# Optimization experiments

Measured on AMD Instinct MI355X. Metric: run time of the kernel, lower is better.

Reference implementation:

```python
import jax, jax.numpy as jnp
import numpy as np
from jax import lax

# Static module config (matches init_kwargs)
KH, KW = 3, 3
SH, SW = 1, 1
PH, PW = 1, 1
DH, DW = 1, 1
DG = 1           # deformable groups
GROUPS = 1


def setup_inputs() -> dict:
    key = jax.random.key(0)
    k1, k2, k3 = jax.random.split(key, 3)
    B, C, H, W = 8, 256, 64, 64
    Co = 256
    K = KH * KW
    x = jax.random.normal(k1, (B, C, H, W), dtype=jnp.float32)
    # offset/mask conv weight: (2+1)*DG*K = 27 output channels; small so offsets are a few pixels
    w_offset = jax.random.normal(k2, (3 * DG * K, C, KH, KW), dtype=jnp.float32) * 0.05
    # main conv weight, uniform(-stdv, stdv) per reset_parameters
    stdv = 1.0 / np.sqrt(C * KH * KW)
    w_conv = jax.random.uniform(k3, (Co, C, KH, KW), dtype=jnp.float32, minval=-stdv, maxval=stdv)
    return {"input_feat": x, "w_offset": w_offset, "w_conv": w_conv}


def _bilinear_gather(x, py, px):
    """x: (B, DG, Cg, H, W); py/px: (B, DG, K, Ho, Wo) float sample coords.
    Returns sampled values (B, DG, Cg, K, Ho, Wo) with zero padding outside."""
    B, dg, Cg, H, W = x.shape
    _, _, K, Ho, Wo = py.shape
    xf = x.reshape(B, dg, Cg, H * W)

    y0 = jnp.floor(py)
    x0 = jnp.floor(px)
    ly = py - y0
    lx = px - x0
    y0i = y0.astype(jnp.int32)
    x0i = x0.astype(jnp.int32)
    y1i = y0i + 1
    x1i = x0i + 1

    def gather(yi, xi):
        valid = (yi >= 0) & (yi < H) & (xi >= 0) & (xi < W)
        idx = jnp.clip(yi, 0, H - 1) * W + jnp.clip(xi, 0, W - 1)  # (B,dg,K,Ho,Wo)
        idx_f = idx.reshape(B, dg, K * Ho * Wo)
        g = jax.vmap(jax.vmap(lambda f, i: jnp.take(f, i, axis=1)))(xf, idx_f)
        return g.reshape(B, dg, Cg, K, Ho, Wo), valid

    g00, v00 = gather(y0i, x0i)
    g01, v01 = gather(y0i, x1i)
    g10, v10 = gather(y1i, x0i)
    g11, v11 = gather(y1i, x1i)

    w00 = ((1 - ly) * (1 - lx) * v00)[:, :, None]
    w01 = ((1 - ly) * lx * v01)[:, :, None]
    w10 = (ly * (1 - lx) * v10)[:, :, None]
    w11 = (ly * lx * v11)[:, :, None]
    return g00 * w00 + g01 * w01 + g10 * w10 + g11 * w11


def _deform_conv(x, w_offset, w_conv):
    B, C, H, W = x.shape
    Co = w_conv.shape[0]
    K = KH * KW
    dn = ("NCHW", "OIHW", "NCHW")

    # offset/mask branch (regular conv)
    om = lax.conv_general_dilated(x, w_offset, (SH, SW), ((PH, PH), (PW, PW)),
                                  rhs_dilation=(DH, DW), dimension_numbers=dn)
    Ho, Wo = om.shape[2], om.shape[3]
    off_y = om[:, : DG * K].reshape(B, DG, K, Ho, Wo)
    off_x = om[:, DG * K: 2 * DG * K].reshape(B, DG, K, Ho, Wo)
    mask = jax.nn.sigmoid(om[:, 2 * DG * K:]).reshape(B, DG, 1, K, Ho, Wo)

    # base sampling grid
    oy = jnp.arange(Ho) * SH - PH                 # (Ho,)
    ox = jnp.arange(Wo) * SW - PW                 # (Wo,)
    ky = (jnp.arange(KH) * DH)[:, None].repeat(KW, 1).reshape(K)  # (K,)
    kx = (jnp.arange(KW) * DW)[None, :].repeat(KH, 0).reshape(K)  # (K,)
    py = ky[None, None, :, None, None] + oy[None, None, None, :, None] + off_y
    px = kx[None, None, :, None, None] + ox[None, None, None, None, :] + off_x

    xg = x.reshape(B, DG, C // DG, H, W)
    sampled = _bilinear_gather(xg, py, px) * mask  # (B,DG,Cg,K,Ho,Wo)

    cols = sampled.reshape(B, C, K, Ho * Wo)
    wk = w_conv.reshape(Co, C, K)
    out = jnp.einsum("bckn,ock->bon", cols, wk)
    return out.reshape(B, Co, Ho, Wo)


def reference(input_feat, w_offset, w_conv):
    return _deform_conv(input_feat, w_offset, w_conv)
```

## Files before the change

kernel.cpp:

```cpp
#include <hip/hip_runtime.h>
#include <hip/hip_bf16.h>

typedef float f32x4 __attribute__((ext_vector_type(4)));
typedef unsigned int u32x4 __attribute__((ext_vector_type(4)));
typedef __bf16 bf16x8 __attribute__((ext_vector_type(8)));

#define NSP 4096
#define KTOT 2304

static __device__ __forceinline__ float bflo(unsigned u) {
  return __builtin_bit_cast(float, u << 16);
}
static __device__ __forceinline__ float bfhi(unsigned u) {
  return __builtin_bit_cast(float, u & 0xffff0000u);
}
static __device__ __forceinline__ unsigned short bfbits(float f) {
  return __builtin_bit_cast(unsigned short, (__bf16)f);
}
static __device__ __forceinline__ unsigned packbf2(float f0, float f1) {
  return (unsigned)bfbits(f0) | ((unsigned)bfbits(f1) << 16);
}
static __device__ __forceinline__ float bf16f(unsigned short h) {
  return __builtin_bit_cast(float, (unsigned)h << 16);
}

static __device__ __forceinline__ void dma16(const unsigned short* g, unsigned short* l) {
  __builtin_amdgcn_global_load_lds(
      (const __attribute__((address_space(1))) unsigned int*)g,
      (__attribute__((address_space(3))) unsigned int*)l, 16, 0, 0);
}

__global__ __launch_bounds__(256) void k_nhwc(const float* __restrict__ x,
                                              unsigned short* __restrict__ XH) {
  const int by = blockIdx.x;
  const int t = threadIdx.x;
  const int xw = t & 63;
  const int cq = t >> 6;
  const float* xp = x + (((by >> 6) * 256 * 64 + (by & 63)) * 64 + xw);
  unsigned short* oh = XH + (by * 64 + xw) * 256;
#pragma unroll
  for (int j8 = 0; j8 < 8; ++j8) {
    const int c0 = cq * 64 + j8 * 8;
    u32x4 vh;
#pragma unroll
    for (int d = 0; d < 4; ++d) {
      float f0 = xp[(c0 + 2 * d) * 4096];
      float f1 = xp[(c0 + 2 * d + 1) * 4096];
      vh[d] = packbf2(f0, f1);
    }
    *(u32x4*)(oh + c0) = vh;
  }
}

__global__ void k_wprep_all(const float* __restrict__ wc, const float* __restrict__ wof,
                            unsigned short* __restrict__ AWL,
                            unsigned short* __restrict__ AF) {
  int idx = blockIdx.x * 256 + threadIdx.x;
  if (idx < 589824) {
    int ks = idx / 16384;
    int e = idx - ks * 16384;
    int row = e >> 6;
    int se = e & 63;
    int offb = (se * 2) ^ ((row & 7) << 4);
    int col = ks * 64 + (offb >> 1);
    int c = col & 255, tap = col >> 8;
    AWL[idx] = bfbits(wc[(row * 256 + c) * 9 + tap]);
  } else {
    int j = idx - 589824;
    if (j < 147456) {
      int skc = j >> 11;
      int r = j & 2047;
      int fi = r >> 9;
      int lane = (r >> 3) & 63;
      int e = r & 7;
      int ks = skc >> 1, kc = skc & 1;
      int tap = ks >> 2, q = ks & 3;
      int mr = lane & 15, ko = (lane >> 4) * 8;
      int m = (fi & 1) * 16 + mr;
      int gcol = tap * 256 + q * 64 + ko + kc * 32 + e;
      int c = gcol & 255;
      int t = gcol >> 8;
      float v = (m < 27) ? wof[(m * 256 + c) * 9 + t] : 0.f;
      unsigned short h = bfbits(v);
      AF[j] = (fi >> 1) ? bfbits(v - bf16f(h)) : h;
    }
  }
}

__global__ __launch_bounds__(256) void k_offc2(const unsigned short* __restrict__ AF,
                                               const unsigned short* __restrict__ XH,
                                               f32x4* __restrict__ W4,
                                               unsigned* __restrict__ C4) {
  __shared__ u32x4 ldsq[1024];
  unsigned char* ldsbase = (unsigned char*)ldsq;
  float* lds32 = (float*)ldsq;

  const int tid = threadIdx.x;
  const int bid = blockIdx.x;
  const int b = bid & 7;
  const int y = bid >> 3;
  const int l = tid & 63;
  const int w = tid >> 6;

  const unsigned short* xb = XH + b * (64 * 64 * 256);
  const int sp = tid >> 2;
  const int qtr = tid & 3;
  const unsigned swb = (unsigned)(sp & 7) << 4;
  const int col = w * 16 + (l & 15);
  const unsigned swc = (unsigned)(col & 7) << 4;

  f32x4 acc0 = (f32x4){0.f, 0.f, 0.f, 0.f};
  f32x4 acc1 = (f32x4){0.f, 0.f, 0.f, 0.f};
  u32x4 v0, v1;

  {
    const int yy = y - 1;
    const int xx = sp - 1;
    const bool valid = ((unsigned)yy < 64u) & ((unsigned)xx < 64u);
    const int yyc = min(max(yy, 0), 63), xxc = min(max(xx, 0), 63);
    const unsigned short* src = xb + ((yyc * 64 + xxc) * 256 + qtr * 16);
    u32x4 z = (u32x4){0u, 0u, 0u, 0u};
    v0 = valid ? *(const u32x4*)src : z;
    v1 = valid ? *(const u32x4*)(src + 8) : z;
    *(u32x4*)(ldsbase + (unsigned)sp * 128u + (((unsigned)(qtr * 32)) ^ swb)) = v0;
    *(u32x4*)(ldsbase + (unsigned)sp * 128u + (((unsigned)(qtr * 32 + 16)) ^ swb)) = v1;
  }

  for (int ks = 0; ks < 36; ++ks) {
    unsigned char* ldsB = ldsbase + (ks & 1) * 8192;
    unsigned char* ldsBn = ldsbase + ((ks & 1) ^ 1) * 8192;
    const bool pf = (ks + 1 < 36);

    if (pf) {
      int tap = (ks + 1) >> 2, q = (ks + 1) & 3;
      int yy = y + tap / 3 - 1, xx = sp + tap % 3 - 1;
      bool valid = ((unsigned)yy < 64u) & ((unsigned)xx < 64u);
      int yyc = min(max(yy, 0), 63), xxc = min(max(xx, 0), 63);
      const unsigned short* src = xb + ((yyc * 64 + xxc) * 256 + q * 64 + qtr * 16);
      u32x4 z = (u32x4){0u, 0u, 0u, 0u};
      v0 = valid ? *(const u32x4*)src : z;
      v1 = valid ? *(const u32x4*)(src + 8) : z;
    }

    asm volatile("s_waitcnt lgkmcnt(0)" ::: "memory");
    __builtin_amdgcn_s_barrier();

    const unsigned short* af = AF + ks * 4096;
#pragma unroll
    for (int kc = 0; kc < 2; ++kc) {
      bf16x8 ah0 = *(const bf16x8*)(af + kc * 2048 + l * 8);
      bf16x8 ah1 = *(const bf16x8*)(af + kc * 2048 + 512 + l * 8);
      bf16x8 al0 = *(const bf16x8*)(af + kc * 2048 + 1024 + l * 8);
      bf16x8 al1 = *(const bf16x8*)(af + kc * 2048 + 1536 + l * 8);
      bf16x8 bh = *(const bf16x8*)(ldsB + (unsigned)col * 128u +
                                   (((unsigned)(kc * 64 + (l >> 4) * 16)) ^ swc));
      acc0 = __builtin_amdgcn_mfma_f32_16x16x32_bf16(ah0, bh, acc0, 0, 0, 0);
      acc1 = __builtin_amdgcn_mfma_f32_16x16x32_bf16(ah1, bh, acc1, 0, 0, 0);
      acc0 = __builtin_amdgcn_mfma_f32_16x16x32_bf16(al0, bh, acc0, 0, 0, 0);
      acc1 = __builtin_amdgcn_mfma_f32_16x16x32_bf16(al1, bh, acc1, 0, 0, 0);
    }

    if (pf) {
      *(u32x4*)(ldsBn + (unsigned)sp * 128u + (((unsigned)(qtr * 32)) ^ swb)) = v0;
      *(u32x4*)(ldsBn + (unsigned)sp * 128u + (((unsigned)(qtr * 32 + 16)) ^ swb)) = v1;
    }
  }

  __syncthreads();
#pragma unroll
  for (int mf = 0; mf < 2; ++mf) {
    f32x4 a = mf ? acc1 : acc0;
#pragma unroll
    for (int r = 0; r < 4; ++r) {
      int m = mf * 16 + (l >> 4) * 4 + r;
      int px = w * 16 + (l & 15);
      lds32[m * 64 + px] = a[r];
    }
  }
  __syncthreads();

#pragma unroll
  for (int it = 0; it < 3; ++it) {
    int idx = tid + it * 256;
    if (idx < 9 * 64) {
      int k = idx >> 6, px = idx & 63;
      float oy = lds32[k * 64 + px];
      float ox = lds32[(9 + k) * 64 + px];
      float lg = lds32[(18 + k) * 64 + px];
      int s = y * 64 + px;
      float py = oy + (float)y - 1.f + (float)(k / 3);
      float pxf = ox + (float)px - 1.f + (float)(k % 3);
      float mk = 1.f / (1.f + __expf(-lg));

      float y0f = floorf(py), x0f = floorf(pxf);
      float ly = py - y0f, lx = pxf - x0f;
      int y0 = (int)y0f, x0 = (int)x0f;
      int y1 = y0 + 1, x1 = x0 + 1;
      float omy = 1.f - ly, omx = 1.f - lx;
      bool y0v = (unsigned)y0 < 64u, y1v = (unsigned)y1 < 64u;
      bool x0v = (unsigned)x0 < 64u, x1v = (unsigned)x1 < 64u;
      f32x4 wv;
      wv[0] = (y0v && x0v) ? omy * omx * mk : 0.f;
      wv[1] = (y0v && x1v) ? omy * lx * mk : 0.f;
      wv[2] = (y1v && x0v) ? ly * omx * mk : 0.f;
      wv[3] = (y1v && x1v) ? ly * lx * mk : 0.f;
      int y0c = min(max(y0, 0), 63), y1c = min(max(y1, 0), 63);
      int x0c = min(max(x0, 0), 63), x1c = min(max(x1, 0), 63);
      unsigned p00 = (unsigned)(y0c * 64 + x0c);
      unsigned p11 = (unsigned)(y1c * 64 + x1c);
      int ci = (b * 9 + k) * NSP + s;
      W4[ci] = wv;
      C4[ci] = p00 | (p11 << 16);
    }
  }
}

struct Bld16 {
  u32x4 g00a, g00b, g01a, g01b, g10a, g10b, g11a, g11b;
  f32x4 wv;
};

static __device__ __forceinline__ void loadMeta(const f32x4* __restrict__ W4,
                                                const unsigned* __restrict__ C4,
                                                int b, int k, int s,
                                                f32x4& wv, unsigned& c4) {
  int ci = (b * 9 + k) * NSP + s;
  wv = W4[ci];
  c4 = C4[ci];
}

static __device__ __forceinline__ void loadCorners(const unsigned short* __restrict__ xb,
                                                   f32x4 wv, unsigned c4, int c0, int bc,
                                                   Bld16& r) {
  r.wv = wv;
  unsigned p00 = c4 & 0xffffu, p11 = c4 >> 16;
  unsigned p01 = (p00 & ~63u) | (p11 & 63u);
  unsigned p10 = (p11 & ~63u) | (p00 & 63u);
  const unsigned short* base = xb + (c0 + bc);
  const unsigned short* q00 = base + (p00 << 8);
  const unsigned short* q01 = base + (p01 << 8);
  const unsigned short* q10 = base + (p10 << 8);
  const unsigned short* q11 = base + (p11 << 8);
  r.g00a = *(const u32x4*)q00;
  r.g00b = *(const u32x4*)(q00 + 8);
  r.g01a = *(const u32x4*)q01;
  r.g01b = *(const u32x4*)(q01 + 8);
  r.g10a = *(const u32x4*)q10;
  r.g10b = *(const u32x4*)(q10 + 8);
  r.g11a = *(const u32x4*)q11;
  r.g11b = *(const u32x4*)(q11 + 8);
}

static __device__ __forceinline__ void blendB16(const Bld16& r, u32x4& o0, u32x4& o1) {
#pragma unroll
  for (int d = 0; d < 4; ++d) {
    float a0 = r.wv[0] * bflo(r.g00a[d]) + r.wv[1] * bflo(r.g01a[d]) +
               r.wv[2] * bflo(r.g10a[d]) + r.wv[3] * bflo(r.g11a[d]);
    float a1 = r.wv[0] * bfhi(r.g00a[d]) + r.wv[1] * bfhi(r.g01a[d]) +
               r.wv[2] * bfhi(r.g10a[d]) + r.wv[3] * bfhi(r.g11a[d]);
    o0[d] = packbf2(a0, a1);
    float b0 = r.wv[0] * bflo(r.g00b[d]) + r.wv[1] * bflo(r.g01b[d]) +
               r.wv[2] * bflo(r.g10b[d]) + r.wv[3] * bflo(r.g11b[d]);
    float b1 = r.wv[0] * bfhi(r.g00b[d]) + r.wv[1] * bfhi(r.g01b[d]) +
               r.wv[2] * bfhi(r.g10b[d]) + r.wv[3] * bfhi(r.g11b[d]);
    o1[d] = packbf2(b0, b1);
  }
}

__global__ __launch_bounds__(512) void k_gemm(const unsigned short* __restrict__ AWL,
                                              const unsigned short* __restrict__ XH,
                                              const f32x4* __restrict__ W4,
                                              const unsigned* __restrict__ C4v,
                                              float* __restrict__ out) {
  __shared__ u32x4 lds2[2][3072];
  unsigned char* ldsbase = (unsigned char*)lds2;

  const int tid = threadIdx.x;
  const int bid = blockIdx.x;
  const int b = bid & 7;
  const int s0 = (bid >> 3) * 128;

  const int l = tid & 63;
  const int w = tid >> 6;
  const int wm = (w >> 1) * 64;
  const int wn = (w & 1) * 64;

  const int bn = tid >> 2;
  const int bc = (tid & 3) * 16;
  const int s = s0 + bn;
  const unsigned swb = (unsigned)(bn & 7) << 4;
  const unsigned short* xb = XH + b * (64 * 64 * 256);

  f32x4 acc[4][4];
#pragma unroll
  for (int i = 0; i < 4; ++i)
#pragma unroll
    for (int j = 0; j < 4; ++j) acc[i][j] = (f32x4){0.f, 0.f, 0.f, 0.f};

  f32x4 mwvA, mwvB;
  unsigned mc4A, mc4B;
  Bld16 bldA, bldB;

  loadMeta(W4, C4v, b, 0, s, mwvA, mc4A);
  loadMeta(W4, C4v, b, 0, s, mwvB, mc4B);
  {
    const unsigned short* g0 = AWL + (w * 4) * 512 + l * 8;
#pragma unroll
    for (int k = 0; k < 4; ++k)
      dma16(g0 + k * 512, (unsigned short*)(ldsbase + (unsigned)(w * 4 + k) * 1024u));
  }
  loadCorners(xb, mwvA, mc4A, 0, bc, bldA);
  loadMeta(W4, C4v, b, 0, s, mwvA, mc4A);
  {
    u32x4 o0, o1;
    blendB16(bldA, o0, o1);
    unsigned char* ldsB = ldsbase + 32768;
    const unsigned bbase = (unsigned)bn * 128u;
    *(u32x4*)(ldsB + bbase + (((unsigned)(bc * 2)) ^ swb)) = o0;
    *(u32x4*)(ldsB + bbase + (((unsigned)(bc * 2 + 16)) ^ swb)) = o1;
  }
  loadCorners(xb, mwvB, mc4B, 64, bc, bldB);

  auto mfma_half = [&](unsigned char* ldsA, unsigned char* ldsB, int H) {
    bf16x8 af[4], bfr[4];
    const unsigned co = (unsigned)(H * 64 + ((l >> 4) * 16));
#pragma unroll
    for (int i = 0; i < 4; ++i) {
      int row = wm + i * 16 + (l & 15);
      af[i] = *(const bf16x8*)(ldsA + (unsigned)row * 128u +
                               (co ^ ((unsigned)(row & 7) << 4)));
    }
#pragma unroll
    for (int j = 0; j < 4; ++j) {
      int col = wn + j * 16 + (l & 15);
      bfr[j] = *(const bf16x8*)(ldsB + (unsigned)col * 128u +
                                (co ^ ((unsigned)(col & 7) << 4)));
    }
#pragma unroll
    for (int i = 0; i < 4; ++i)
#pragma unroll
      for (int j = 0; j < 4; ++j)
        acc[i][j] = __builtin_amdgcn_mfma_f32_16x16x32_bf16(af[i], bfr[j],
                                                            acc[i][j], 0, 0, 0);
  };

  auto gstep = [&](int KS, Bld16& bldI, f32x4& mwvI, unsigned& mc4I,
                   f32x4& mwvO, unsigned& mc4O, Bld16& bldU) {
    const int cur = KS & 1;
    unsigned char* ldsA = ldsbase + cur * 49152;
    unsigned char* ldsB = ldsA + 32768;
    unsigned char* ldsAn = ldsbase + (cur ^ 1) * 49152;
    unsigned char* ldsBn = ldsAn + 32768;

    __syncthreads();

    if (KS + 1 < 36) {
      const unsigned short* g0 = AWL + (KS + 1) * 16384 + (w * 4) * 512 + l * 8;
#pragma unroll
      for (int k = 0; k < 4; ++k)
        dma16(g0 + k * 512, (unsigned short*)(ldsAn + (unsigned)(w * 4 + k) * 1024u));
    }

    __builtin_amdgcn_s_setprio(1);
    mfma_half(ldsA, ldsB, 0);
    __builtin_amdgcn_s_setprio(0);

    if (KS + 2 < 36)
      loadCorners(xb, mwvI, mc4I, ((KS + 2) & 3) << 6, bc, bldI);
    if (KS + 3 < 36)
      loadMeta(W4, C4v, b, (KS + 3) >> 2, s, mwvO, mc4O);

    __builtin_amdgcn_s_setprio(1);
    mfma_half(ldsA, ldsB, 1);
    __builtin_amdgcn_s_setprio(0);

    if (KS + 1 < 36) {
      u32x4 o0, o1;
      blendB16(bldU, o0, o1);
      const unsigned bbase = (unsigned)bn * 128u;
      *(u32x4*)(ldsBn + bbase + (((unsigned)(bc * 2)) ^ swb)) = o0;
      *(u32x4*)(ldsBn + bbase + (((unsigned)(bc * 2 + 16)) ^ swb)) = o1;
    }
  };

  for (int ks2 = 0; ks2 < 36; ks2 += 2) {
    gstep(ks2, bldA, mwvA, mc4A, mwvB, mc4B, bldB);
    gstep(ks2 + 1, bldB, mwvB, mc4B, mwvA, mc4A, bldA);
  }

  const int cn2 = l & 15;
  const int r0 = (l >> 4) * 4;
#pragma unroll
  for (int i = 0; i < 4; ++i) {
#pragma unroll
    for (int j = 0; j < 4; ++j) {
      int sc = s0 + wn + j * 16 + cn2;
#pragma unroll
      for (int r = 0; r < 4; ++r) {
        int o = wm + i * 16 + r0 + r;
        out[((b * 256 + o) << 12) + sc] = acc[i][j][r];
      }
    }
  }
}

extern "C" void kernel_launch(void* const* d_in, const int* in_sizes, int n_in,
                              void* d_out, int out_size, void* d_ws, size_t ws_size,
                              hipStream_t stream) {
  const float* x = (const float*)d_in[0];
  const float* wof = (const float*)d_in[1];
  const float* wc = (const float*)d_in[2];
  float* out = (float*)d_out;
  char* ws = (char*)d_ws;

  unsigned short* XH = (unsigned short*)(ws);
  unsigned short* AWL = (unsigned short*)(ws + 16777216);
  unsigned short* AF = (unsigned short*)(ws + 17956864);
  f32x4* W4 = (f32x4*)(ws + 18251776);
  unsigned* C4 = (unsigned*)(ws + 22970368);

  k_nhwc<<<512, 256, 0, stream>>>(x, XH);
  k_wprep_all<<<2880, 256, 0, stream>>>(wc, wof, AWL, AF);
  k_offc2<<<512, 256, 0, stream>>>(AF, XH, W4, C4);
  k_gemm<<<256, 512, 0, stream>>>(AWL, XH, W4, C4, out);
}
```

Baseline: 114.6 us.

## Split GEMM K dimension across two blocks with atomic accumulation

Splits the 36-step K loop of the deformable-conv GEMM into two halves handled by separate blocks, doubling the grid from 256 to 512 blocks so the 256-CU device is better filled. The output is zeroed with a memset and partial sums are combined with float atomicAdd. The B tile now uses a single LDS buffer guarded by an extra barrier, which shrinks LDS use to allow more blocks per CU. The cost is atomic traffic on the output, an extra memset, one more barrier per step, and nondeterministic summation order.

```diff
diff --git a/kernel.cpp b/kernel.cpp
--- a/kernel.cpp
+++ b/kernel.cpp
@@ -267,18 +267,20 @@
   }
 }
 
-__global__ __launch_bounds__(512) void k_gemm(const unsigned short* __restrict__ AWL,
-                                              const unsigned short* __restrict__ XH,
-                                              const f32x4* __restrict__ W4,
-                                              const unsigned* __restrict__ C4v,
-                                              float* __restrict__ out) {
-  __shared__ u32x4 lds2[2][3072];
+__global__ __launch_bounds__(512, 4) void k_gemm(const unsigned short* __restrict__ AWL,
+                                                 const unsigned short* __restrict__ XH,
+                                                 const f32x4* __restrict__ W4,
+                                                 const unsigned* __restrict__ C4v,
+                                                 float* __restrict__ out) {
+  __shared__ u32x4 lds2[5120];
   unsigned char* ldsbase = (unsigned char*)lds2;
+  unsigned char* ldsB = ldsbase + 65536;
 
   const int tid = threadIdx.x;
   const int bid = blockIdx.x;
   const int b = bid & 7;
-  const int s0 = (bid >> 3) * 128;
+  const int s0 = ((bid >> 3) & 31) * 128;
+  const int kb = (bid >> 8) * 18;
 
   const int l = tid & 63;
   const int w = tid >> 6;
@@ -301,27 +303,26 @@
   unsigned mc4A, mc4B;
   Bld16 bldA, bldB;
 
-  loadMeta(W4, C4v, b, 0, s, mwvA, mc4A);
-  loadMeta(W4, C4v, b, 0, s, mwvB, mc4B);
+  loadMeta(W4, C4v, b, kb >> 2, s, mwvA, mc4A);
+  loadMeta(W4, C4v, b, (kb + 1) >> 2, s, mwvB, mc4B);
   {
-    const unsigned short* g0 = AWL + (w * 4) * 512 + l * 8;
+    const unsigned short* g0 = AWL + kb * 16384 + (w * 4) * 512 + l * 8;
 #pragma unroll
     for (int k = 0; k < 4; ++k)
       dma16(g0 + k * 512, (unsigned short*)(ldsbase + (unsigned)(w * 4 + k) * 1024u));
   }
-  loadCorners(xb, mwvA, mc4A, 0, bc, bldA);
-  loadMeta(W4, C4v, b, 0, s, mwvA, mc4A);
+  loadCorners(xb, mwvA, mc4A, (kb & 3) << 6, bc, bldA);
+  loadMeta(W4, C4v, b, (kb + 2) >> 2, s, mwvA, mc4A);
   {
     u32x4 o0, o1;
     blendB16(bldA, o0, o1);
-    unsigned char* ldsB = ldsbase + 32768;
     const unsigned bbase = (unsigned)bn * 128u;
     *(u32x4*)(ldsB + bbase + (((unsigned)(bc * 2)) ^ swb)) = o0;
     *(u32x4*)(ldsB + bbase + (((unsigned)(bc * 2 + 16)) ^ swb)) = o1;
   }
-  loadCorners(xb, mwvB, mc4B, 64, bc, bldB);
-
-  auto mfma_half = [&](unsigned char* ldsA, unsigned char* ldsB, int H) {
+  loadCorners(xb, mwvB, mc4B, ((kb + 1) & 3) << 6, bc, bldB);
+
+  auto mfma_half = [&](unsigned char* ldsA, int H) {
     bf16x8 af[4], bfr[4];
     const unsigned co = (unsigned)(H * 64 + ((l >> 4) * 16));
 #pragma unroll
@@ -346,44 +347,45 @@
 
   auto gstep = [&](int KS, Bld16& bldI, f32x4& mwvI, unsigned& mc4I,
                    f32x4& mwvO, unsigned& mc4O, Bld16& bldU) {
-    const int cur = KS & 1;
-    unsigned char* ldsA = ldsbase + cur * 49152;
-    unsigned char* ldsB = ldsA + 32768;
-    unsigned char* ldsAn = ldsbase + (cur ^ 1) * 49152;
-    unsigned char* ldsBn = ldsAn + 32768;
+    const int G = kb + KS;
+    unsigned char* ldsA = ldsbase + (KS & 1) * 32768;
+    unsigned char* ldsAn = ldsbase + ((KS & 1) ^ 1) * 32768;
 
     __syncthreads();
 
-    if (KS + 1 < 36) {
-      const unsigned short* g0 = AWL + (KS + 1) * 16384 + (w * 4) * 512 + l * 8;
+    if (KS + 1 < 18) {
+      const unsigned short* g0 = AWL + (G + 1) * 16384 + (w * 4) * 512 + l * 8;
 #pragma unroll
       for (int k = 0; k < 4; ++k)
         dma16(g0 + k * 512, (unsigned short*)(ldsAn + (unsigned)(w * 4 + k) * 1024u));
     }
 
     __builtin_amdgcn_s_setprio(1);
-    mfma_half(ldsA, ldsB, 0);
+    mfma_half(ldsA, 0);
     __builtin_amdgcn_s_setprio(0);
 
-    if (KS + 2 < 36)
-      loadCorners(xb, mwvI, mc4I, ((KS + 2) & 3) << 6, bc, bldI);
-    if (KS + 3 < 36)
-      loadMeta(W4, C4v, b, (KS + 3) >> 2, s, mwvO, mc4O);
+    if (KS + 2 < 18)
+      loadCorners(xb, mwvI, mc4I, ((G + 2) & 3) << 6, bc, bldI);
+    if (KS + 3 < 18)
+      loadMeta(W4, C4v, b, (G + 3) >> 2, s, mwvO, mc4O);
 
     __builtin_amdgcn_s_setprio(1);
-    mfma_half(ldsA, ldsB, 1);
+    mfma_half(ldsA, 1);
     __builtin_amdgcn_s_setprio(0);
 
-    if (KS + 1 < 36) {
+    asm volatile("s_waitcnt lgkmcnt(0)" ::: "memory");
+    __builtin_amdgcn_s_barrier();
+
+    if (KS + 1 < 18) {
       u32x4 o0, o1;
       blendB16(bldU, o0, o1);
       const unsigned bbase = (unsigned)bn * 128u;
-      *(u32x4*)(ldsBn + bbase + (((unsigned)(bc * 2)) ^ swb)) = o0;
-      *(u32x4*)(ldsBn + bbase + (((unsigned)(bc * 2 + 16)) ^ swb)) = o1;
+      *(u32x4*)(ldsB + bbase + (((unsigned)(bc * 2)) ^ swb)) = o0;
+      *(u32x4*)(ldsB + bbase + (((unsigned)(bc * 2 + 16)) ^ swb)) = o1;
     }
   };
 
-  for (int ks2 = 0; ks2 < 36; ks2 += 2) {
+  for (int ks2 = 0; ks2 < 18; ks2 += 2) {
     gstep(ks2, bldA, mwvA, mc4A, mwvB, mc4B, bldB);
     gstep(ks2 + 1, bldB, mwvB, mc4B, mwvA, mc4A, bldA);
   }
@@ -398,7 +400,7 @@
 #pragma unroll
       for (int r = 0; r < 4; ++r) {
         int o = wm + i * 16 + r0 + r;
-        out[((b * 256 + o) << 12) + sc] = acc[i][j][r];
+        atomicAdd(&out[((b * 256 + o) << 12) + sc], acc[i][j][r]);
       }
     }
   }
@@ -419,8 +421,9 @@
   f32x4* W4 = (f32x4*)(ws + 18251776);
   unsigned* C4 = (unsigned*)(ws + 22970368);
 
+  hipMemsetAsync(d_out, 0, (size_t)out_size * 4, stream);
   k_nhwc<<<512, 256, 0, stream>>>(x, XH);
   k_wprep_all<<<2880, 256, 0, stream>>>(wc, wof, AWL, AF);
   k_offc2<<<512, 256, 0, stream>>>(AF, XH, W4, C4);
-  k_gemm<<<256, 512, 0, stream>>>(AWL, XH, W4, C4, out);
-}
+  k_gemm<<<512, 512, 0, stream>>>(AWL, XH, W4, C4, out);
+}
```

Result: slower. 407.4 us (+255.6%).

## Split gemm block into MFMA consumer waves and dedicated gather-blend producer waves

Applied to the files above, without the earlier changes.

The fused deformable-gather GEMM now launches 768 threads per block: 8 waves only run MFMA on the LDS tiles and issue the weight DMA, while 4 extra producer waves gather the bilinear corners, blend them, and write the next B tile into double-buffered LDS. The goal is to take the gather latency and blend ALU work off the MFMA waves so the two overlap through warp specialization. The cost is a larger block with more registers per block, a producer that now covers 32 channels per thread with a shallower one-step prefetch, and a reorganised LDS layout.

```diff
diff --git a/kernel.cpp b/kernel.cpp
--- a/kernel.cpp
+++ b/kernel.cpp
@@ -215,81 +215,33 @@
   }
 }
 
-struct Bld16 {
-  u32x4 g00a, g00b, g01a, g01b, g10a, g10b, g11a, g11b;
-  f32x4 wv;
-};
-
-static __device__ __forceinline__ void loadMeta(const f32x4* __restrict__ W4,
-                                                const unsigned* __restrict__ C4,
-                                                int b, int k, int s,
-                                                f32x4& wv, unsigned& c4) {
-  int ci = (b * 9 + k) * NSP + s;
-  wv = W4[ci];
-  c4 = C4[ci];
-}
-
-static __device__ __forceinline__ void loadCorners(const unsigned short* __restrict__ xb,
-                                                   f32x4 wv, unsigned c4, int c0, int bc,
-                                                   Bld16& r) {
-  r.wv = wv;
-  unsigned p00 = c4 & 0xffffu, p11 = c4 >> 16;
-  unsigned p01 = (p00 & ~63u) | (p11 & 63u);
-  unsigned p10 = (p11 & ~63u) | (p00 & 63u);
-  const unsigned short* base = xb + (c0 + bc);
-  const unsigned short* q00 = base + (p00 << 8);
-  const unsigned short* q01 = base + (p01 << 8);
-  const unsigned short* q10 = base + (p10 << 8);
-  const unsigned short* q11 = base + (p11 << 8);
-  r.g00a = *(const u32x4*)q00;
-  r.g00b = *(const u32x4*)(q00 + 8);
-  r.g01a = *(const u32x4*)q01;
-  r.g01b = *(const u32x4*)(q01 + 8);
-  r.g10a = *(const u32x4*)q10;
-  r.g10b = *(const u32x4*)(q10 + 8);
-  r.g11a = *(const u32x4*)q11;
-  r.g11b = *(const u32x4*)(q11 + 8);
-}
-
-static __device__ __forceinline__ void blendB16(const Bld16& r, u32x4& o0, u32x4& o1) {
-#pragma unroll
-  for (int d = 0; d < 4; ++d) {
-    float a0 = r.wv[0] * bflo(r.g00a[d]) + r.wv[1] * bflo(r.g01a[d]) +
-               r.wv[2] * bflo(r.g10a[d]) + r.wv[3] * bflo(r.g11a[d]);
-    float a1 = r.wv[0] * bfhi(r.g00a[d]) + r.wv[1] * bfhi(r.g01a[d]) +
-               r.wv[2] * bfhi(r.g10a[d]) + r.wv[3] * bfhi(r.g11a[d]);
-    o0[d] = packbf2(a0, a1);
-    float b0 = r.wv[0] * bflo(r.g00b[d]) + r.wv[1] * bflo(r.g01b[d]) +
-               r.wv[2] * bflo(r.g10b[d]) + r.wv[3] * bflo(r.g11b[d]);
-    float b1 = r.wv[0] * bfhi(r.g00b[d]) + r.wv[1] * bfhi(r.g01b[d]) +
-               r.wv[2] * bfhi(r.g10b[d]) + r.wv[3] * bfhi(r.g11b[d]);
-    o1[d] = packbf2(b0, b1);
-  }
-}
-
-__global__ __launch_bounds__(512) void k_gemm(const unsigned short* __restrict__ AWL,
-                                              const unsigned short* __restrict__ XH,
-                                              const f32x4* __restrict__ W4,
-                                              const unsigned* __restrict__ C4v,
-                                              float* __restrict__ out) {
-  __shared__ u32x4 lds2[2][3072];
+__global__ __launch_bounds__(768, 3) void k_gemm(const unsigned short* __restrict__ AWL,
+                                                 const unsigned short* __restrict__ XH,
+                                                 const f32x4* __restrict__ W4,
+                                                 const unsigned* __restrict__ C4v,
+                                                 float* __restrict__ out) {
+  __shared__ u32x4 lds2[6144];
   unsigned char* ldsbase = (unsigned char*)lds2;
+  unsigned char* ldsBbase = ldsbase + 65536;
 
   const int tid = threadIdx.x;
   const int bid = blockIdx.x;
   const int b = bid & 7;
   const int s0 = (bid >> 3) * 128;
+  const unsigned short* xb = XH + b * (64 * 64 * 256);
+
+  const bool isProd = tid >= 512;
 
   const int l = tid & 63;
   const int w = tid >> 6;
   const int wm = (w >> 1) * 64;
   const int wn = (w & 1) * 64;
 
-  const int bn = tid >> 2;
-  const int bc = (tid & 3) * 16;
-  const int s = s0 + bn;
-  const unsigned swb = (unsigned)(bn & 7) << 4;
-  const unsigned short* xb = XH + b * (64 * 64 * 256);
+  const int pt = tid - 512;
+  const int px = pt >> 1;
+  const int chb = (pt & 1) * 32;
+  const int ps = s0 + px;
+  const unsigned swb = (unsigned)(px & 7) << 4;
 
   f32x4 acc[4][4];
 #pragma unroll
@@ -297,108 +249,154 @@
 #pragma unroll
     for (int j = 0; j < 4; ++j) acc[i][j] = (f32x4){0.f, 0.f, 0.f, 0.f};
 
-  f32x4 mwvA, mwvB;
-  unsigned mc4A, mc4B;
-  Bld16 bldA, bldB;
-
-  loadMeta(W4, C4v, b, 0, s, mwvA, mc4A);
-  loadMeta(W4, C4v, b, 0, s, mwvB, mc4B);
-  {
+  u32x4 c00[4], c01[4], c10[4], c11[4];
+  f32x4 mwv;
+  unsigned mc4 = 0u;
+
+  if (!isProd) {
     const unsigned short* g0 = AWL + (w * 4) * 512 + l * 8;
 #pragma unroll
     for (int k = 0; k < 4; ++k)
       dma16(g0 + k * 512, (unsigned short*)(ldsbase + (unsigned)(w * 4 + k) * 1024u));
-  }
-  loadCorners(xb, mwvA, mc4A, 0, bc, bldA);
-  loadMeta(W4, C4v, b, 0, s, mwvA, mc4A);
-  {
-    u32x4 o0, o1;
-    blendB16(bldA, o0, o1);
-    unsigned char* ldsB = ldsbase + 32768;
-    const unsigned bbase = (unsigned)bn * 128u;
-    *(u32x4*)(ldsB + bbase + (((unsigned)(bc * 2)) ^ swb)) = o0;
-    *(u32x4*)(ldsB + bbase + (((unsigned)(bc * 2 + 16)) ^ swb)) = o1;
-  }
-  loadCorners(xb, mwvB, mc4B, 64, bc, bldB);
-
-  auto mfma_half = [&](unsigned char* ldsA, unsigned char* ldsB, int H) {
-    bf16x8 af[4], bfr[4];
-    const unsigned co = (unsigned)(H * 64 + ((l >> 4) * 16));
+  } else {
+    {
+      int ci = (b * 9 + 0) * NSP + ps;
+      mwv = W4[ci];
+      mc4 = C4v[ci];
+    }
+    {
+      unsigned p00 = mc4 & 0xffffu, p11 = mc4 >> 16;
+      unsigned p01 = (p00 & ~63u) | (p11 & 63u);
+      unsigned p10 = (p11 & ~63u) | (p00 & 63u);
+      const unsigned short* base = xb + chb;
+      const unsigned short* q00 = base + (p00 << 8);
+      const unsigned short* q01 = base + (p01 << 8);
+      const unsigned short* q10 = base + (p10 << 8);
+      const unsigned short* q11 = base + (p11 << 8);
+#pragma unroll
+      for (int q = 0; q < 4; ++q) {
+        c00[q] = *(const u32x4*)(q00 + q * 8);
+        c01[q] = *(const u32x4*)(q01 + q * 8);
+        c10[q] = *(const u32x4*)(q10 + q * 8);
+        c11[q] = *(const u32x4*)(q11 + q * 8);
+      }
+#pragma unroll
+      for (int q = 0; q < 4; ++q) {
+        u32x4 o;
+#pragma unroll
+        for (int d = 0; d < 4; ++d) {
+          float a0 = mwv[0] * bflo(c00[q][d]) + mwv[1] * bflo(c01[q][d]) +
+                     mwv[2] * bflo(c10[q][d]) + mwv[3] * bflo(c11[q][d]);
+          float a1 = mwv[0] * bfhi(c00[q][d]) + mwv[1] * bfhi(c01[q][d]) +
+                     mwv[2] * bfhi(c10[q][d]) + mwv[3] * bfhi(c11[q][d]);
+          o[d] = packbf2(a0, a1);
+        }
+        *(u32x4*)(ldsBbase + (unsigned)px * 128u +
+                  (((unsigned)(chb * 2 + q * 16)) ^ swb)) = o;
+      }
+    }
+    {
+      int ci = (b * 9 + 0) * NSP + ps;
+      mwv = W4[ci];
+      mc4 = C4v[ci];
+    }
+  }
+
+  for (int t = 0; t < 36; ++t) {
+    __syncthreads();
+
+    if (!isProd) {
+      if (t + 1 < 36) {
+        const unsigned short* g0 = AWL + (t + 1) * 16384 + (w * 4) * 512 + l * 8;
+        unsigned char* ldsAn = ldsbase + ((t + 1) & 1) * 32768;
+#pragma unroll
+        for (int k = 0; k < 4; ++k)
+          dma16(g0 + k * 512, (unsigned short*)(ldsAn + (unsigned)(w * 4 + k) * 1024u));
+      }
+      unsigned char* ldsA = ldsbase + (t & 1) * 32768;
+      unsigned char* ldsB = ldsBbase + (t & 1) * 16384;
+      __builtin_amdgcn_s_setprio(1);
+#pragma unroll
+      for (int H = 0; H < 2; ++H) {
+        bf16x8 af[4], bfr[4];
+        const unsigned co = (unsigned)(H * 64 + ((l >> 4) * 16));
+#pragma unroll
+        for (int i = 0; i < 4; ++i) {
+          int row = wm + i * 16 + (l & 15);
+          af[i] = *(const bf16x8*)(ldsA + (unsigned)row * 128u +
+                                   (co ^ ((unsigned)(row & 7) << 4)));
+        }
+#pragma unroll
+        for (int j = 0; j < 4; ++j) {
+          int col = wn + j * 16 + (l & 15);
+          bfr[j] = *(const bf16x8*)(ldsB + (unsigned)col * 128u +
+                                    (co ^ ((unsigned)(col & 7) << 4)));
+        }
+#pragma unroll
+        for (int i = 0; i < 4; ++i)
+#pragma unroll
+          for (int j = 0; j < 4; ++j)
+            acc[i][j] = __builtin_amdgcn_mfma_f32_16x16x32_bf16(af[i], bfr[j],
+                                                                acc[i][j], 0, 0, 0);
+      }
+      __builtin_amdgcn_s_setprio(0);
+    } else {
+      f32x4 wvS = mwv;
+      if (t + 1 < 36) {
+        unsigned p00 = mc4 & 0xffffu, p11 = mc4 >> 16;
+        unsigned p01 = (p00 & ~63u) | (p11 & 63u);
+        unsigned p10 = (p11 & ~63u) | (p00 & 63u);
+        const unsigned short* base = xb + (((t + 1) & 3) << 6) + chb;
+        const unsigned short* q00 = base + (p00 << 8);
+        const unsigned short* q01 = base + (p01 << 8);
+        const unsigned short* q10 = base + (p10 << 8);
+        const unsigned short* q11 = base + (p11 << 8);
+#pragma unroll
+        for (int q = 0; q < 4; ++q) {
+          c00[q] = *(const u32x4*)(q00 + q * 8);
+          c01[q] = *(const u32x4*)(q01 + q * 8);
+          c10[q] = *(const u32x4*)(q10 + q * 8);
+          c11[q] = *(const u32x4*)(q11 + q * 8);
+        }
+      }
+      if (t + 2 < 36) {
+        int ci = (b * 9 + ((t + 2) >> 2)) * NSP + ps;
+        mwv = W4[ci];
+        mc4 = C4v[ci];
+      }
+      if (t + 1 < 36) {
+        unsigned char* ldsBn = ldsBbase + ((t + 1) & 1) * 16384;
+#pragma unroll
+        for (int q = 0; q < 4; ++q) {
+          u32x4 o;
+#pragma unroll
+          for (int d = 0; d < 4; ++d) {
+            float a0 = wvS[0] * bflo(c00[q][d]) + wvS[1] * bflo(c01[q][d]) +
+                       wvS[2] * bflo(c10[q][d]) + wvS[3] * bflo(c11[q][d]);
+            float a1 = wvS[0] * bfhi(c00[q][d]) + wvS[1] * bfhi(c01[q][d]) +
+                       wvS[2] * bfhi(c10[q][d]) + wvS[3] * bfhi(c11[q][d]);
+            o[d] = packbf2(a0, a1);
+          }
+          *(u32x4*)(ldsBn + (unsigned)px * 128u +
+                    (((unsigned)(chb * 2 + q * 16)) ^ swb)) = o;
+        }
+      }
+    }
+  }
+
+  if (!isProd) {
+    const int cn2 = l & 15;
+    const int r0 = (l >> 4) * 4;
 #pragma unroll
     for (int i = 0; i < 4; ++i) {
-      int row = wm + i * 16 + (l & 15);
-      af[i] = *(const bf16x8*)(ldsA + (unsigned)row * 128u +
-                               (co ^ ((unsigned)(row & 7) << 4)));
-    }
-#pragma unroll
-    for (int j = 0; j < 4; ++j) {
-      int col = wn + j * 16 + (l & 15);
-      bfr[j] = *(const bf16x8*)(ldsB + (unsigned)col * 128u +
-                                (co ^ ((unsigned)(col & 7) << 4)));
-    }
-#pragma unroll
-    for (int i = 0; i < 4; ++i)
-#pragma unroll
-      for (int j = 0; j < 4; ++j)
-        acc[i][j] = __builtin_amdgcn_mfma_f32_16x16x32_bf16(af[i], bfr[j],
-                                                            acc[i][j], 0, 0, 0);
-  };
-
-  auto gstep = [&](int KS, Bld16& bldI, f32x4& mwvI, unsigned& mc4I,
-                   f32x4& mwvO, unsigned& mc4O, Bld16& bldU) {
-    const int cur = KS & 1;
-    unsigned char* ldsA = ldsbase + cur * 49152;
-    unsigned char* ldsB = ldsA + 32768;
-    unsigned char* ldsAn = ldsbase + (cur ^ 1) * 49152;
-    unsigned char* ldsBn = ldsAn + 32768;
-
-    __syncthreads();
-
-    if (KS + 1 < 36) {
-      const unsigned short* g0 = AWL + (KS + 1) * 16384 + (w * 4) * 512 + l * 8;
-#pragma unroll
-      for (int k = 0; k < 4; ++k)
-        dma16(g0 + k * 512, (unsigned short*)(ldsAn + (unsigned)(w * 4 + k) * 1024u));
-    }
-
-    __builtin_amdgcn_s_setprio(1);
-    mfma_half(ldsA, ldsB, 0);
-    __builtin_amdgcn_s_setprio(0);
-
-    if (KS + 2 < 36)
-      loadCorners(xb, mwvI, mc4I, ((KS + 2) & 3) << 6, bc, bldI);
-    if (KS + 3 < 36)
-      loadMeta(W4, C4v, b, (KS + 3) >> 2, s, mwvO, mc4O);
-
-    __builtin_amdgcn_s_setprio(1);
-    mfma_half(ldsA, ldsB, 1);
-    __builtin_amdgcn_s_setprio(0);
-
-    if (KS + 1 < 36) {
-      u32x4 o0, o1;
-      blendB16(bldU, o0, o1);
-      const unsigned bbase = (unsigned)bn * 128u;
-      *(u32x4*)(ldsBn + bbase + (((unsigned)(bc * 2)) ^ swb)) = o0;
-      *(u32x4*)(ldsBn + bbase + (((unsigned)(bc * 2 + 16)) ^ swb)) = o1;
-    }
-  };
-
-  for (int ks2 = 0; ks2 < 36; ks2 += 2) {
-    gstep(ks2, bldA, mwvA, mc4A, mwvB, mc4B, bldB);
-    gstep(ks2 + 1, bldB, mwvB, mc4B, mwvA, mc4A, bldA);
-  }
-
-  const int cn2 = l & 15;
-  const int r0 = (l >> 4) * 4;
-#pragma unroll
-  for (int i = 0; i < 4; ++i) {
-#pragma unroll
-    for (int j = 0; j < 4; ++j) {
-      int sc = s0 + wn + j * 16 + cn2;
-#pragma unroll
-      for (int r = 0; r < 4; ++r) {
-        int o = wm + i * 16 + r0 + r;
-        out[((b * 256 + o) << 12) + sc] = acc[i][j][r];
+#pragma unroll
+      for (int j = 0; j < 4; ++j) {
+        int sc = s0 + wn + j * 16 + cn2;
+#pragma unroll
+        for (int r = 0; r < 4; ++r) {
+          int o = wm + i * 16 + r0 + r;
+          out[((b * 256 + o) << 12) + sc] = acc[i][j][r];
+        }
       }
     }
   }
@@ -422,5 +420,5 @@
   k_nhwc<<<512, 256, 0, stream>>>(x, XH);
   k_wprep_all<<<2880, 256, 0, stream>>>(wc, wof, AWL, AF);
   k_offc2<<<512, 256, 0, stream>>>(AF, XH, W4, C4);
-  k_gemm<<<256, 512, 0, stream>>>(AWL, XH, W4, C4, out);
-}
+  k_gemm<<<256, 768, 0, stream>>>(AWL, XH, W4, C4, out);
+}
```

Measured after the change: 140.2 us. +22.4%, slower.
